# Performance work log

Hardware: AMD Instinct MI355X
Metric: run time of the kernel (lower is better)

The kernel has to match this reference:

```python
import jax, jax.numpy as jnp
import numpy as np


def _rotated_kernels(kernel, n_or):
    """Nearest-neighbour rotated copies of the kernel.

    kernel: [C, kOr, kH, kW] -> returns [n_or, C, kOr, kH, kW] where slice t is the
    kernel sampled at R_{2*pi*t/n_or}(y', x') about the kernel center; rotated
    coordinates that fall outside the kernel grid contribute zero.
    """
    C, kOr, kH, kW = kernel.shape
    cy = (kH - 1) / 2.0
    cx = (kW - 1) / 2.0
    ang = 2.0 * jnp.pi * jnp.arange(n_or, dtype=jnp.float32) / n_or
    ca = jnp.cos(ang)[:, None, None]  # [n_or,1,1]
    sa = jnp.sin(ang)[:, None, None]
    yy = jnp.arange(kH, dtype=jnp.float32)[:, None] - cy  # [kH,1]
    xx = jnp.arange(kW, dtype=jnp.float32)[None, :] - cx  # [1,kW]
    # rotate grid points by angle theta
    ys = sa * xx + ca * yy  # [n_or,kH,kW]
    xs = ca * xx - sa * yy
    iy = jnp.round(ys + cy).astype(jnp.int32)
    ix = jnp.round(xs + cx).astype(jnp.int32)
    mask = ((iy >= 0) & (iy < kH) & (ix >= 0) & (ix < kW)).astype(kernel.dtype)
    iyc = jnp.clip(iy, 0, kH - 1)
    ixc = jnp.clip(ix, 0, kW - 1)
    rot = kernel[:, :, iyc, ixc]            # [C,kOr,n_or,kH,kW] (gather)
    rot = rot * mask[None, None]            # zero out-of-grid samples
    return jnp.transpose(rot, (2, 0, 1, 3, 4))  # [n_or,C,kOr,kH,kW]


def setup_inputs() -> dict:
    key = jax.random.key(0)
    k1, k2 = jax.random.split(key)
    B, C, Or, H, W = 8, 32, 8, 128, 128
    kOr, kH, kW = 8, 5, 5
    x = jax.random.normal(k1, (B, C, Or, H, W), dtype=jnp.float32)
    # module parameter: uniform(-1, 1) per reset_parameters()
    kernel = jax.random.uniform(k2, (C, kOr, kH, kW), minval=-1.0, maxval=1.0,
                                dtype=jnp.float32)
    return {"x": x, "kernel": kernel}


def reference(x, kernel):
    """SE(2) linear (depthwise) group convolution.

    out[b,c,t,y,x] = sum_{t',y',x'} x[b,c,(t+t')%Or, y+y', x+x']
                     * kernel[c, t', NN(R_{2pi t/Or}(y', x'))]
    with centered, zero-padded spatial offsets ('SAME').
    """
    B, C, Or, H, W = x.shape
    _, kOr, kH, kW = kernel.shape
    rotk = _rotated_kernels(kernel, Or)  # [Or,C,kOr,kH,kW]
    dn = ('NCHW', 'OIHW', 'NCHW')
    out = jnp.zeros((B, C * Or, H, W), dtype=x.dtype)
    for tp in range(kOr):  # small fixed orientation-offset loop
        xs = jnp.roll(x, -tp, axis=2).reshape(B, C * Or, H, W)  # circular wrap in Or
        k = jnp.transpose(rotk[:, :, tp], (1, 0, 2, 3)).reshape(C * Or, 1, kH, kW)
        out = out + jax.lax.conv_general_dilated(
            xs, k, window_strides=(1, 1), padding='SAME',
            feature_group_count=C * Or, dimension_numbers=dn)
    return out.reshape(B, C, Or, H, W)
```

## Files before the change

### kernel.cpp

```cpp
#include <hip/hip_runtime.h>


typedef short bf16x8 __attribute__((ext_vector_type(8)));
typedef float f32x4 __attribute__((ext_vector_type(4)));

#define EPIL_TS 1092
#define EPIL_RP 68

__device__ inline unsigned short f2bf(float f) {
    unsigned int u = __float_as_uint(f);
    u += 0x7fffu + ((u >> 16) & 1u);
    return (unsigned short)(u >> 16);
}
__device__ inline unsigned pk2(float a, float b) {
    return (unsigned)f2bf(a) | ((unsigned)f2bf(b) << 16);
}

__device__ __constant__ float CA8[8] = {1.0f, 0.70710678f, 0.0f, -0.70710678f,
                                        -1.0f, -0.70710678f, 0.0f, 0.70710678f};
__device__ __constant__ float SA8[8] = {0.0f, 0.70710678f, 1.0f, 0.70710678f,
                                        0.0f, -0.70710678f, -1.0f, -0.70710678f};

__device__ inline float rot_w(const float* __restrict__ kern, int c, int t,
                              int o, int dy, int dx) {
    float ca = CA8[t], sa = SA8[t];
    float xx = (float)dx - 2.0f, yy = (float)dy - 2.0f;
    int iy = (int)rintf(sa * xx + ca * yy + 2.0f);
    int ix = (int)rintf(ca * xx - sa * yy + 2.0f);
    if (iy >= 0 && iy < 5 && ix >= 0 && ix < 5) {
        int tp = (o - t) & 7;
        return kern[(c * 8 + tp) * 25 + iy * 5 + ix];
    }
    return 0.0f;
}

__global__ __launch_bounds__(256)
void build_w2(const float* __restrict__ kern, unsigned short* __restrict__ wtab) {
    int e = blockIdx.x * 256 + threadIdx.x;
    if (e >= 131072) return;
    int o   = e & 7;
    int tr  = (e >> 3) & 31;
    int n16 = (e >> 8) & 15;
    int c   = e >> 12;
    int t   = n16 & 7, dlt = n16 >> 3;
    float w = 0.0f;
    if (tr < 30) {
        int dyr = tr / 5, dx = tr - 5 * dyr;
        int dy  = dyr - dlt;
        if (dy >= 0 && dy < 5) w = rot_w(kern, c, t, o, dy, dx);
    }
    wtab[e] = f2bf(w);
}

template <bool TAB>
__global__ __launch_bounds__(256)
void se2_mfma(const float* __restrict__ x, const float* __restrict__ kern,
              const unsigned short* __restrict__ wtab, float* __restrict__ out) {
    __shared__ __align__(16) float ldsbuf[8 * EPIL_TS];
    unsigned short* stage = reinterpret_cast<unsigned short*>(ldsbuf);
    float* epil = ldsbuf;

    const int bid = (blockIdx.x & 7) * 512 + (blockIdx.x >> 3);
    const int xh2 = bid & 1;
    const int ys  = (bid >> 1) & 7;
    const int bc  = bid >> 4;
    const int c   = bc & 31;
    const int X0  = xh2 * 64, Y0 = ys * 16;
    const int tid = threadIdx.x;

    const int lane = tid & 63;
    const int wv   = tid >> 6;
    const int g    = lane >> 4;
    const int m16  = lane & 15;

    const float* xbase = x + (size_t)bc * 131072;

    auto loadch = [&](int e, float (&v)[8]) {
        int r = e / 68, col = e - r * 68;
        int gy = Y0 - 2 + r, gx = X0 - 2 + col;
        if (gy >= 0 && gy < 128 && gx >= 0 && gx < 128) {
            const float* src = xbase + gy * 128 + gx;
#pragma unroll
            for (int o = 0; o < 8; ++o) v[o] = src[o * 16384];
        } else {
#pragma unroll
            for (int o = 0; o < 8; ++o) v[o] = 0.0f;
        }
    };
    auto packch = [&](int e, const float (&v)[8]) {
        *reinterpret_cast<uint4*>(&stage[e * 8]) =
            make_uint4(pk2(v[0], v[1]), pk2(v[2], v[3]),
                       pk2(v[4], v[5]), pk2(v[6], v[7]));
    };

    float sA[8], sB[8];
    loadch(tid, sA);
    loadch(tid + 256, sB);

    bf16x8 wfrag[8];
    int    tapoff[8];
#pragma unroll
    for (int cc = 0; cc < 8; ++cc) {
        int tr  = cc * 4 + g;
        int trc = tr < 30 ? tr : 29;
        int dyr = trc / 5, dx = trc - 5 * dyr;
        tapoff[cc] = (dyr * 68 + dx) * 8;
        if constexpr (TAB)
            wfrag[cc] = *reinterpret_cast<const bf16x8*>(
                &wtab[((c * 16 + m16) * 32 + tr) * 8]);
    }

    if constexpr (!TAB) {
        unsigned short* ldsw = stage + 12288;
        for (int e = tid; e < 4096; e += 256) {
            int o = e & 7, tr = (e >> 3) & 31, n16 = e >> 8;
            int t = n16 & 7, dlt = n16 >> 3;
            float w = 0.0f;
            if (tr < 30) {
                int dyr = tr / 5, dx = tr - 5 * dyr;
                int dy  = dyr - dlt;
                if (dy >= 0 && dy < 5) w = rot_w(kern, c, t, o, dy, dx);
            }
            ldsw[e] = f2bf(w);
        }
        __syncthreads();
#pragma unroll
        for (int cc = 0; cc < 8; ++cc)
            wfrag[cc] = *reinterpret_cast<const bf16x8*>(
                &ldsw[(m16 * 32 + cc * 4 + g) * 8]);
        __syncthreads();
    }

    packch(tid, sA);
    packch(tid + 256, sB);
    loadch(tid + 512, sA);
    loadch(tid + 768, sB);
    packch(tid + 512, sA);
    packch(tid + 768, sB);
    loadch(tid + 1024, sA);
    if (tid < 80) loadch(tid + 1280, sB);
    packch(tid + 1024, sA);
    if (tid < 80) packch(tid + 1280, sB);
    __syncthreads();

    f32x4 acc[8];
#pragma unroll
    for (int s = 0; s < 8; ++s) {
        acc[s] = (f32x4){0.f, 0.f, 0.f, 0.f};
        const int yl = wv * 4 + (s >> 2) * 2;
        const int baseS = (yl * 68 + (s & 3) * 16 + m16) * 8;
#pragma unroll
        for (int cc = 0; cc < 8; ++cc) {
            bf16x8 xf = *reinterpret_cast<const bf16x8*>(&stage[baseS + tapoff[cc]]);
            acc[s] = __builtin_amdgcn_mfma_f32_16x16x32_bf16(xf, wfrag[cc], acc[s], 0, 0, 0);
        }
    }
    __syncthreads();

    const int t_o = m16 & 7, dlt = m16 >> 3;
#pragma unroll
    for (int s = 0; s < 8; ++s) {
        int y = wv * 4 + (s >> 2) * 2 + dlt;
        int xx = (s & 3) * 16 + g * 4;
        *reinterpret_cast<f32x4*>(&epil[t_o * EPIL_TS + y * EPIL_RP + xx]) = acc[s];
    }
    __syncthreads();

    const int xq   = lane & 15;
    const int yloc = lane >> 4;
    float* outb = out + (size_t)bc * 131072;
#pragma unroll
    for (int j = 0; j < 8; ++j) {
        int t = wv * 2 + (j & 1);
        int y = (j >> 1) * 4 + yloc;
        f32x4 v = *reinterpret_cast<const f32x4*>(
            &epil[t * EPIL_TS + y * EPIL_RP + xq * 4]);
        __builtin_nontemporal_store(v, reinterpret_cast<f32x4*>(
            outb + (size_t)t * 16384 + (size_t)(Y0 + y) * 128 + X0 + xq * 4));
    }
}

extern "C" void kernel_launch(void* const* d_in, const int* in_sizes, int n_in,
                              void* d_out, int out_size, void* d_ws, size_t ws_size,
                              hipStream_t stream) {
    const float* x    = (const float*)d_in[0];
    const float* kern = (const float*)d_in[1];
    float* out = (float*)d_out;
    dim3 block(256);
    if (ws_size >= 131072 * sizeof(unsigned short)) {
        unsigned short* wtab = (unsigned short*)d_ws;
        build_w2<<<dim3(512), block, 0, stream>>>(kern, wtab);
        se2_mfma<true><<<dim3(4096), block, 0, stream>>>(x, kern, wtab, out);
    } else {
        se2_mfma<false><<<dim3(4096), block, 0, stream>>>(x, kern, nullptr, out);
    }
}
```

Measured before the change: 53.92 us.

## Issue all input loads upfront and remove epilogue block barrier via wave-local remap

All six staging load batches are issued before weight fragment setup, so more global reads are in flight before packing into LDS. The epilogue readback is remapped so each wave only reads rows it wrote itself, which allows dropping a __syncthreads. This raises register pressure from holding 48 floats of staged input, which could reduce occupancy.

New measurement: 52.35 us. 2.9% less time.

```diff
diff --git a/kernel.cpp b/kernel.cpp
--- a/kernel.cpp
+++ b/kernel.cpp
@@ -93,9 +93,13 @@
                        pk2(v[4], v[5]), pk2(v[6], v[7]));
     };
 
-    float sA[8], sB[8];
-    loadch(tid, sA);
-    loadch(tid + 256, sB);
+    float v0[8], v1[8], v2[8], v3[8], v4[8], v5[8];
+    loadch(tid, v0);
+    loadch(tid + 256, v1);
+    loadch(tid + 512, v2);
+    loadch(tid + 768, v3);
+    loadch(tid + 1024, v4);
+    if (tid < 80) loadch(tid + 1280, v5);
 
     bf16x8 wfrag[8];
     int    tapoff[8];
@@ -131,16 +135,12 @@
         __syncthreads();
     }
 
-    packch(tid, sA);
-    packch(tid + 256, sB);
-    loadch(tid + 512, sA);
-    loadch(tid + 768, sB);
-    packch(tid + 512, sA);
-    packch(tid + 768, sB);
-    loadch(tid + 1024, sA);
-    if (tid < 80) loadch(tid + 1280, sB);
-    packch(tid + 1024, sA);
-    if (tid < 80) packch(tid + 1280, sB);
+    packch(tid, v0);
+    packch(tid + 256, v1);
+    packch(tid + 512, v2);
+    packch(tid + 768, v3);
+    packch(tid + 1024, v4);
+    if (tid < 80) packch(tid + 1280, v5);
     __syncthreads();
 
     f32x4 acc[8];
@@ -160,19 +160,19 @@
     const int t_o = m16 & 7, dlt = m16 >> 3;
 #pragma unroll
     for (int s = 0; s < 8; ++s) {
-        int y = wv * 4 + (s >> 2) * 2 + dlt;
+        int y  = wv * 4 + (s >> 2) * 2 + dlt;
         int xx = (s & 3) * 16 + g * 4;
         *reinterpret_cast<f32x4*>(&epil[t_o * EPIL_TS + y * EPIL_RP + xx]) = acc[s];
     }
-    __syncthreads();
 
-    const int xq   = lane & 15;
-    const int yloc = lane >> 4;
     float* outb = out + (size_t)bc * 131072;
 #pragma unroll
     for (int j = 0; j < 8; ++j) {
-        int t = wv * 2 + (j & 1);
-        int y = (j >> 1) * 4 + yloc;
+        int idx = j * 64 + lane;
+        int xq  = idx & 15;
+        int y4  = (idx >> 4) & 3;
+        int t   = idx >> 6;
+        int y   = wv * 4 + y4;
         f32x4 v = *reinterpret_cast<const f32x4*>(
             &epil[t * EPIL_TS + y * EPIL_RP + xq * 4]);
         __builtin_nontemporal_store(v, reinterpret_cast<f32x4*>(
```
